# Optimization experiments

Measured on AMD Instinct MI355X. Metric: run time of the kernel, lower is better.

The kernel has to match this reference:

```python
import jax, jax.numpy as jnp
import numpy as np

H = 256  # hidden size for both encoder and decoder

def gru_cell(x, h, Wih, Whh, bih, bhh):
    # PyTorch nn.GRU cell: gates ordered (r, z, n)
    gi = x @ Wih.T + bih            # [N, 3H]
    gh = h @ Whh.T + bhh            # [N, 3H]
    ir, iz, inn = jnp.split(gi, 3, axis=-1)
    hr, hz, hn = jnp.split(gh, 3, axis=-1)
    r = jax.nn.sigmoid(ir + hr)
    z = jax.nn.sigmoid(iz + hz)
    n = jnp.tanh(inn + r * hn)
    return (1.0 - z) * n + z * h


def setup_inputs() -> dict:
    key = jax.random.key(0)
    ks = jax.random.split(key, 16)
    s = 0.05
    inp = {
        'x': jax.random.normal(ks[0], (32768, 15, 4), jnp.float32),
        'enc_embed_W': jax.random.normal(ks[1], (H, 4), jnp.float32) * s,
        'enc_embed_b': jax.random.normal(ks[2], (H,), jnp.float32) * s,
        'enc_Wih': jax.random.normal(ks[3], (3 * H, H), jnp.float32) * s,
        'enc_Whh': jax.random.normal(ks[4], (3 * H, H), jnp.float32) * s,
        'enc_bih': jax.random.normal(ks[5], (3 * H,), jnp.float32) * s,
        'enc_bhh': jax.random.normal(ks[6], (3 * H,), jnp.float32) * s,
        'dec_embed_W': jax.random.normal(ks[7], (H, H), jnp.float32) * s,
        'dec_embed_b': jax.random.normal(ks[8], (H,), jnp.float32) * s,
        'dec_Wih': jax.random.normal(ks[9], (3 * H, H), jnp.float32) * s,
        'dec_Whh': jax.random.normal(ks[10], (3 * H, H), jnp.float32) * s,
        'dec_bih': jax.random.normal(ks[11], (3 * H,), jnp.float32) * s,
        'dec_bhh': jax.random.normal(ks[12], (3 * H,), jnp.float32) * s,
        'out_W': jax.random.normal(ks[13], (4, H), jnp.float32) * s,
        'out_b': jax.random.normal(ks[14], (4,), jnp.float32) * s,
        'pred_len': 45,
    }
    return inp


def reference(x, enc_embed_W, enc_embed_b, enc_Wih, enc_Whh, enc_bih, enc_bhh,
              dec_embed_W, dec_embed_b, dec_Wih, dec_Whh, dec_bih, dec_bhh,
              out_W, out_b, pred_len):
    N = x.shape[0]
    # enc_embed: Linear + ReLU
    traj_feats = jax.nn.relu(jnp.einsum('nti,hi->nth', x, enc_embed_W) + enc_embed_b)
    # Encoder GRU over time (batch_first); we only need the final hidden state.
    h0 = jnp.zeros((N, H), x.dtype)

    def enc_step(h, xt):
        h = gru_cell(xt, h, enc_Wih, enc_Whh, enc_bih, enc_bhh)
        return h, None

    h_enc, _ = jax.lax.scan(enc_step, h0, jnp.swapaxes(traj_feats, 0, 1))

    dec_in0 = jax.nn.relu(h_enc @ dec_embed_W.T + dec_embed_b)

    def dec_step(carry, _):
        h, dec_in = carry
        h = gru_cell(dec_in, h, dec_Wih, dec_Whh, dec_bih, dec_bhh)
        out_t = h @ out_W.T + out_b                     # [N, 4]
        dec_in = jax.nn.relu(h @ dec_embed_W.T + dec_embed_b)
        return (h, dec_in), out_t

    _, outs = jax.lax.scan(dec_step, (h_enc, dec_in0), None, length=pred_len)
    return jnp.swapaxes(outs, 0, 1)  # [N, pred_len, 4]
```

## Files before the change

kernel.cpp:

```cpp
#include <hip/hip_runtime.h>
#include <hip/hip_bf16.h>
#include <hip/hip_fp16.h>

#define HD    256
#define TENC  15
#define PLEN  45
#define MROW  64
#define NTHR  512
#define NBLK  (32768 / MROW)

typedef __attribute__((ext_vector_type(16))) float f32x16;
typedef __attribute__((ext_vector_type(8)))  short bf16x8;

#define MFMA32 __builtin_amdgcn_mfma_f32_32x32x16_bf16

__device__ __forceinline__ unsigned short f2bf(float f) {
    union { float f; unsigned int u; } v; v.f = f;
    unsigned int r = v.u + 0x7FFF + ((v.u >> 16) & 1);
    return (unsigned short)(r >> 16);
}

__device__ __forceinline__ float fast_sig(float x) {
    float e = __builtin_amdgcn_exp2f(-1.44269504088896f * x);
    return __builtin_amdgcn_rcpf(1.f + e);
}
__device__ __forceinline__ float fast_tanh(float x) {
    float e = __builtin_amdgcn_exp2f(-2.88539008177793f * x);
    return (1.f - e) * __builtin_amdgcn_rcpf(1.f + e);
}

__global__ void xpose_w_kernel(const float* __restrict__ src,
                               unsigned short* __restrict__ dst, int n_gcols) {
    int t = blockIdx.x * blockDim.x + threadIdx.x;
    if (t >= n_gcols * 32) return;
    int gcol = t >> 5, c8 = t & 31;
    int kk = c8 >> 1, hi = c8 & 1;
    const float* s = src + (size_t)gcol * HD + c8 * 8;
    int seg = gcol >> 8, gc = gcol & 255;
    size_t d = (size_t)seg * 65536 +
               ((size_t)(((gc >> 5) * 16 + kk) * 64 + hi * 32 + (gc & 31))) * 8;
    unsigned short v[8];
    #pragma unroll
    for (int e = 0; e < 8; ++e) v[e] = f2bf(s[e]);
    *(bf16x8*)(dst + d) = *(bf16x8*)v;
}

__global__ void xpose_ow_kernel(const float* __restrict__ src,
                                unsigned short* __restrict__ dst) {
    int t = blockIdx.x * blockDim.x + threadIdx.x;
    if (t >= 32 * 32) return;
    int gcol = t >> 5, c8 = t & 31;
    int kk = c8 >> 1, hi = c8 & 1;
    unsigned short v[8];
    if (gcol < 4) {
        const float* s = src + (size_t)gcol * HD + c8 * 8;
        #pragma unroll
        for (int e = 0; e < 8; ++e) v[e] = f2bf(s[e]);
    } else {
        #pragma unroll
        for (int e = 0; e < 8; ++e) v[e] = 0;
    }
    size_t d = ((size_t)(kk * 64 + hi * 32 + gcol)) * 8;
    *(bf16x8*)(dst + d) = *(bf16x8*)v;
}

__device__ __forceinline__ int swz(int row, int col) {
    return row * 512 + ((((col >> 3) ^ row) & 31) << 4) + ((col & 7) << 1);
}

__global__ __launch_bounds__(NTHR, 2) void gru_main(
    const float* __restrict__ x,
    const float* __restrict__ eW, const float* __restrict__ eb,
    const unsigned short* __restrict__ encWih, const unsigned short* __restrict__ encWhh,
    const float* __restrict__ enc_bih, const float* __restrict__ enc_bhh,
    const unsigned short* __restrict__ decEW, const float* __restrict__ dec_eb,
    const unsigned short* __restrict__ decWih, const unsigned short* __restrict__ decWhh,
    const float* __restrict__ dec_bih, const float* __restrict__ dec_bhh,
    const unsigned short* __restrict__ outWt, const float* __restrict__ outb,
    float* __restrict__ out)
{
    __shared__ __align__(16) unsigned short ls_a[MROW * HD];
    __shared__ __align__(16) unsigned short ls_h[MROW * HD];
    __shared__ float ls_ew[HD * 4];
    __shared__ float ls_eb[HD];
    __shared__ float ls_bias[4 * HD];
    __shared__ float ls_deb[HD];

    const int tid   = threadIdx.x;
    const int lane  = tid & 63;
    const int wv    = tid >> 6;
    const int rowA  = lane & 31;
    const int hi    = lane >> 5;
    const int col   = wv * 32 + rowA;
    const int nbase = blockIdx.x * MROW;

    for (int i = tid; i < HD * 4; i += NTHR) ls_ew[i] = eW[i];
    if (tid < HD) {
        ls_eb[tid]            = eb[tid];
        ls_bias[tid]          = enc_bih[tid] + enc_bhh[tid];
        ls_bias[HD + tid]     = enc_bih[HD + tid] + enc_bhh[HD + tid];
        ls_bias[2 * HD + tid] = enc_bih[2 * HD + tid];
        ls_bias[3 * HD + tid] = enc_bhh[2 * HD + tid];
    }
    for (int i = tid; i < MROW * HD / 2; i += NTHR) ((unsigned int*)ls_h)[i] = 0u;

    __half2 hpk[16];
    #pragma unroll
    for (int i = 0; i < 16; ++i) hpk[i] = __floats2half2_rn(0.f, 0.f);

    float bR, bZ, bN, bH;

    f32x16 accR0, accR1, accZ0, accZ1, accN10, accN11, accN20, accN21;

    const char* pa = (const char*)ls_a + rowA * 512;
    const char* ph = (const char*)ls_h + rowA * 512;

    auto bcast = [](float v) {
        f32x16 a;
        #pragma unroll
        for (int i = 0; i < 16; ++i) a[i] = v;
        return a;
    };

    auto gates = [&](const unsigned short* Wi, const unsigned short* Wh) {
        accR0 = bcast(bR);  accR1 = accR0;
        accZ0 = bcast(bZ);  accZ1 = accZ0;
        accN10 = bcast(bN); accN11 = accN10;
        accN20 = bcast(bH); accN21 = accN20;
        const unsigned short* bi = Wi + wv * 8192 + lane * 8;
        const unsigned short* bh = Wh + wv * 8192 + lane * 8;
        #pragma unroll 2
        for (int kk = 0; kk < 16; ++kk) {
            const int sh = (((kk * 2 + hi) ^ rowA) & 31) << 4;
            bf16x8 ax0 = *(const bf16x8*)(pa + sh);
            bf16x8 ax1 = *(const bf16x8*)(pa + 16384 + sh);
            bf16x8 ah0 = *(const bf16x8*)(ph + sh);
            bf16x8 ah1 = *(const bf16x8*)(ph + 16384 + sh);
            const unsigned short* ki = bi + kk * 512;
            const unsigned short* kh = bh + kk * 512;
            bf16x8 bri = *(const bf16x8*)(ki);
            bf16x8 bzi = *(const bf16x8*)(ki + 65536);
            bf16x8 bni = *(const bf16x8*)(ki + 131072);
            bf16x8 brh = *(const bf16x8*)(kh);
            bf16x8 bzh = *(const bf16x8*)(kh + 65536);
            bf16x8 bnh = *(const bf16x8*)(kh + 131072);
            accR0  = MFMA32(ax0, bri, accR0, 0, 0, 0);
            accR1  = MFMA32(ax1, bri, accR1, 0, 0, 0);
            accZ0  = MFMA32(ax0, bzi, accZ0, 0, 0, 0);
            accZ1  = MFMA32(ax1, bzi, accZ1, 0, 0, 0);
            accN10 = MFMA32(ax0, bni, accN10, 0, 0, 0);
            accN11 = MFMA32(ax1, bni, accN11, 0, 0, 0);
            accR0  = MFMA32(ah0, brh, accR0, 0, 0, 0);
            accR1  = MFMA32(ah1, brh, accR1, 0, 0, 0);
            accZ0  = MFMA32(ah0, bzh, accZ0, 0, 0, 0);
            accZ1  = MFMA32(ah1, bzh, accZ1, 0, 0, 0);
            accN20 = MFMA32(ah0, bnh, accN20, 0, 0, 0);
            accN21 = MFMA32(ah1, bnh, accN21, 0, 0, 0);
        }
    };

    auto upd_tile = [&](f32x16& aR, f32x16& aZ, f32x16& aN1, f32x16& aN2, int rt) {
        #pragma unroll
        for (int q = 0; q < 16; q += 2) {
            float2 hv = __half22float2(hpk[rt * 8 + (q >> 1)]);
            float r0 = fast_sig(aR[q]);
            float z0 = fast_sig(aZ[q]);
            float n0 = fast_tanh(fmaf(r0, aN2[q], aN1[q]));
            float h0 = fmaf(z0, hv.x - n0, n0);
            float r1 = fast_sig(aR[q + 1]);
            float z1 = fast_sig(aZ[q + 1]);
            float n1 = fast_tanh(fmaf(r1, aN2[q + 1], aN1[q + 1]));
            float h1 = fmaf(z1, hv.y - n1, n1);
            hpk[rt * 8 + (q >> 1)] = __floats2half2_rn(h0, h1);
        }
    };

    auto write_h = [&]() {
        #pragma unroll
        for (int rt = 0; rt < 2; ++rt)
            #pragma unroll
            for (int q = 0; q < 16; q += 2) {
                float2 hv = __half22float2(hpk[rt * 8 + (q >> 1)]);
                int row = rt * 32 + (q & 3) + ((q >> 2) << 3) + (hi << 2);
                *(unsigned short*)((char*)ls_h + swz(row, col))     = f2bf(hv.x);
                *(unsigned short*)((char*)ls_h + swz(row + 1, col)) = f2bf(hv.y);
            }
    };

    auto embed_step = [&](int t) {
        int row = tid & 63;
        int c0  = (tid >> 6) * 32;
        const float4 xv = *(const float4*)(x + ((size_t)(nbase + row) * TENC + t) * 4);
        #pragma unroll 8
        for (int j = 0; j < 32; ++j) {
            int c = c0 + j;
            const float* wp = &ls_ew[c * 4];
            float v = fmaf(xv.x, wp[0], fmaf(xv.y, wp[1],
                      fmaf(xv.z, wp[2], fmaf(xv.w, wp[3], ls_eb[c]))));
            *(unsigned short*)((char*)ls_a + swz(row, c)) = f2bf(fmaxf(v, 0.f));
        }
    };

    float deb;

    auto dec_embed = [&]() {
        f32x16 o0 = bcast(deb), o1 = o0;
        const unsigned short* be = decEW + wv * 8192 + lane * 8;
        #pragma unroll 2
        for (int kk = 0; kk < 16; ++kk) {
            const int sh = (((kk * 2 + hi) ^ rowA) & 31) << 4;
            bf16x8 a0 = *(const bf16x8*)(ph + sh);
            bf16x8 a1 = *(const bf16x8*)(ph + 16384 + sh);
            bf16x8 b = *(const bf16x8*)(be + kk * 512);
            o0 = MFMA32(a0, b, o0, 0, 0, 0);
            o1 = MFMA32(a1, b, o1, 0, 0, 0);
        }
        #pragma unroll
        for (int rt = 0; rt < 2; ++rt) {
            const f32x16& o = rt ? o1 : o0;
            #pragma unroll
            for (int q = 0; q < 16; ++q) {
                int row = rt * 32 + (q & 3) + ((q >> 2) << 3) + (hi << 2);
                *(unsigned short*)((char*)ls_a + swz(row, col)) =
                    f2bf(fmaxf(o[q], 0.f));
            }
        }
    };

    float bb;

    auto out_layer = [&](int t) {
        if ((wv & 3) == 0) {
            const int rt = wv >> 2;
            f32x16 o = bcast(bb);
            const unsigned short* bo = outWt + lane * 8;
            #pragma unroll 2
            for (int kk = 0; kk < 16; ++kk) {
                const int sh = (((kk * 2 + hi) ^ rowA) & 31) << 4;
                bf16x8 a = *(const bf16x8*)(ph + rt * 16384 + sh);
                bf16x8 b = *(const bf16x8*)(bo + kk * 512);
                o = MFMA32(a, b, o, 0, 0, 0);
            }
            if (rowA < 4) {
                #pragma unroll
                for (int q = 0; q < 16; ++q) {
                    int row = rt * 32 + (q & 3) + ((q >> 2) << 3) + (hi << 2);
                    out[((size_t)(nbase + row) * PLEN + t) * 4 + rowA] = o[q];
                }
            }
        }
    };

    __syncthreads();
    bR = ls_bias[col];
    bZ = ls_bias[HD + col];
    bN = ls_bias[2 * HD + col];
    bH = ls_bias[3 * HD + col];
    embed_step(0);
    __syncthreads();

    for (int t = 0; t < TENC; ++t) {
        gates(encWih, encWhh);
        upd_tile(accR0, accZ0, accN10, accN20, 0);
        upd_tile(accR1, accZ1, accN11, accN21, 1);
        __syncthreads();
        write_h();
        if (t + 1 < TENC) embed_step(t + 1);
        __syncthreads();
    }

    if (tid < HD) {
        ls_bias[tid]          = dec_bih[tid] + dec_bhh[tid];
        ls_bias[HD + tid]     = dec_bih[HD + tid] + dec_bhh[HD + tid];
        ls_bias[2 * HD + tid] = dec_bih[2 * HD + tid];
        ls_bias[3 * HD + tid] = dec_bhh[2 * HD + tid];
        ls_deb[tid]           = dec_eb[tid];
    }
    __syncthreads();
    bR = ls_bias[col];
    bZ = ls_bias[HD + col];
    bN = ls_bias[2 * HD + col];
    bH = ls_bias[3 * HD + col];
    deb = ls_deb[col];
    bb  = (rowA < 4) ? outb[rowA] : 0.f;
    dec_embed();
    __syncthreads();

    for (int t = 0; t < PLEN; ++t) {
        gates(decWih, decWhh);
        upd_tile(accR0, accZ0, accN10, accN20, 0);
        upd_tile(accR1, accZ1, accN11, accN21, 1);
        __syncthreads();
        write_h();
        __syncthreads();
        dec_embed();
        __syncthreads();
        out_layer(t);
    }
}

extern "C" void kernel_launch(void* const* d_in, const int* in_sizes, int n_in,
                              void* d_out, int out_size, void* d_ws, size_t ws_size,
                              hipStream_t stream) {
    const float* x       = (const float*)d_in[0];
    const float* eW      = (const float*)d_in[1];
    const float* eb      = (const float*)d_in[2];
    const float* encWihf = (const float*)d_in[3];
    const float* encWhhf = (const float*)d_in[4];
    const float* enc_bih = (const float*)d_in[5];
    const float* enc_bhh = (const float*)d_in[6];
    const float* decEWf  = (const float*)d_in[7];
    const float* dec_eb  = (const float*)d_in[8];
    const float* decWihf = (const float*)d_in[9];
    const float* decWhhf = (const float*)d_in[10];
    const float* dec_bih = (const float*)d_in[11];
    const float* dec_bhh = (const float*)d_in[12];
    const float* outW    = (const float*)d_in[13];
    const float* outb    = (const float*)d_in[14];

    unsigned short* ws = (unsigned short*)d_ws;
    unsigned short* bWih_e = ws;
    unsigned short* bWhh_e = ws + 196608;
    unsigned short* bWih_d = ws + 2 * 196608;
    unsigned short* bWhh_d = ws + 3 * 196608;
    unsigned short* bEW_d  = ws + 4 * 196608;
    unsigned short* bOWt   = ws + 4 * 196608 + 65536;

    const int t1 = 768 * 32;
    const int t2 = 256 * 32;
    xpose_w_kernel<<<(t1 + 255) / 256, 256, 0, stream>>>(encWihf, bWih_e, 768);
    xpose_w_kernel<<<(t1 + 255) / 256, 256, 0, stream>>>(encWhhf, bWhh_e, 768);
    xpose_w_kernel<<<(t1 + 255) / 256, 256, 0, stream>>>(decWihf, bWih_d, 768);
    xpose_w_kernel<<<(t1 + 255) / 256, 256, 0, stream>>>(decWhhf, bWhh_d, 768);
    xpose_w_kernel<<<(t2 + 255) / 256, 256, 0, stream>>>(decEWf,  bEW_d,  256);
    xpose_ow_kernel<<<4, 256, 0, stream>>>(outW, bOWt);

    gru_main<<<NBLK, NTHR, 0, stream>>>(
        x, eW, eb, bWih_e, bWhh_e, enc_bih, enc_bhh,
        bEW_d, dec_eb, bWih_d, bWhh_d, dec_bih, dec_bhh,
        bOWt, outb, (float*)d_out);
}
```

Baseline: 2.279 ms.

## Double rows per block, split gate GEMMs into two passes, switch to fp16 MFMA

Each block now handles 128 rows instead of 64, so each weight fragment loaded from global memory feeds four MFMA row tiles instead of two. To hold the larger tile within registers, the gate computation is split into two passes: the first computes r and the hidden-side n term, combined in a mid step, and the second computes z and the input-side n term. Weights and activations move from bf16 to fp16, which removes the manual bf16 rounding and lets h be written straight from its half-packed registers. The cost is twice the LDS per block, half as many blocks, reuse of the A operands across both passes, and fp16 range limits.

```diff
diff --git a/kernel.cpp b/kernel.cpp
--- a/kernel.cpp
+++ b/kernel.cpp
@@ -5,20 +5,14 @@
 #define HD    256
 #define TENC  15
 #define PLEN  45
-#define MROW  64
+#define MROW  128
 #define NTHR  512
 #define NBLK  (32768 / MROW)
 
-typedef __attribute__((ext_vector_type(16))) float f32x16;
-typedef __attribute__((ext_vector_type(8)))  short bf16x8;
-
-#define MFMA32 __builtin_amdgcn_mfma_f32_32x32x16_bf16
-
-__device__ __forceinline__ unsigned short f2bf(float f) {
-    union { float f; unsigned int u; } v; v.f = f;
-    unsigned int r = v.u + 0x7FFF + ((v.u >> 16) & 1);
-    return (unsigned short)(r >> 16);
-}
+typedef __attribute__((ext_vector_type(16))) float     f32x16;
+typedef __attribute__((ext_vector_type(8)))  _Float16  f16x8;
+
+#define MFMAH __builtin_amdgcn_mfma_f32_32x32x16_f16
 
 __device__ __forceinline__ float fast_sig(float x) {
     float e = __builtin_amdgcn_exp2f(-1.44269504088896f * x);
@@ -30,7 +24,7 @@
 }
 
 __global__ void xpose_w_kernel(const float* __restrict__ src,
-                               unsigned short* __restrict__ dst, int n_gcols) {
+                               _Float16* __restrict__ dst, int n_gcols) {
     int t = blockIdx.x * blockDim.x + threadIdx.x;
     if (t >= n_gcols * 32) return;
     int gcol = t >> 5, c8 = t & 31;
@@ -39,29 +33,29 @@
     int seg = gcol >> 8, gc = gcol & 255;
     size_t d = (size_t)seg * 65536 +
                ((size_t)(((gc >> 5) * 16 + kk) * 64 + hi * 32 + (gc & 31))) * 8;
-    unsigned short v[8];
+    _Float16 v[8];
     #pragma unroll
-    for (int e = 0; e < 8; ++e) v[e] = f2bf(s[e]);
-    *(bf16x8*)(dst + d) = *(bf16x8*)v;
+    for (int e = 0; e < 8; ++e) v[e] = (_Float16)s[e];
+    *(f16x8*)(dst + d) = *(f16x8*)v;
 }
 
 __global__ void xpose_ow_kernel(const float* __restrict__ src,
-                                unsigned short* __restrict__ dst) {
+                                _Float16* __restrict__ dst) {
     int t = blockIdx.x * blockDim.x + threadIdx.x;
     if (t >= 32 * 32) return;
     int gcol = t >> 5, c8 = t & 31;
     int kk = c8 >> 1, hi = c8 & 1;
-    unsigned short v[8];
+    _Float16 v[8];
     if (gcol < 4) {
         const float* s = src + (size_t)gcol * HD + c8 * 8;
         #pragma unroll
-        for (int e = 0; e < 8; ++e) v[e] = f2bf(s[e]);
+        for (int e = 0; e < 8; ++e) v[e] = (_Float16)s[e];
     } else {
         #pragma unroll
-        for (int e = 0; e < 8; ++e) v[e] = 0;
+        for (int e = 0; e < 8; ++e) v[e] = (_Float16)0.f;
     }
     size_t d = ((size_t)(kk * 64 + hi * 32 + gcol)) * 8;
-    *(bf16x8*)(dst + d) = *(bf16x8*)v;
+    *(f16x8*)(dst + d) = *(f16x8*)v;
 }
 
 __device__ __forceinline__ int swz(int row, int col) {
@@ -71,16 +65,16 @@
 __global__ __launch_bounds__(NTHR, 2) void gru_main(
     const float* __restrict__ x,
     const float* __restrict__ eW, const float* __restrict__ eb,
-    const unsigned short* __restrict__ encWih, const unsigned short* __restrict__ encWhh,
+    const _Float16* __restrict__ encWih, const _Float16* __restrict__ encWhh,
     const float* __restrict__ enc_bih, const float* __restrict__ enc_bhh,
-    const unsigned short* __restrict__ decEW, const float* __restrict__ dec_eb,
-    const unsigned short* __restrict__ decWih, const unsigned short* __restrict__ decWhh,
+    const _Float16* __restrict__ decEW, const float* __restrict__ dec_eb,
+    const _Float16* __restrict__ decWih, const _Float16* __restrict__ decWhh,
     const float* __restrict__ dec_bih, const float* __restrict__ dec_bhh,
-    const unsigned short* __restrict__ outWt, const float* __restrict__ outb,
+    const _Float16* __restrict__ outWt, const float* __restrict__ outb,
     float* __restrict__ out)
 {
-    __shared__ __align__(16) unsigned short ls_a[MROW * HD];
-    __shared__ __align__(16) unsigned short ls_h[MROW * HD];
+    __shared__ __align__(16) char ls_a[MROW * 512];
+    __shared__ __align__(16) char ls_h[MROW * 512];
     __shared__ float ls_ew[HD * 4];
     __shared__ float ls_eb[HD];
     __shared__ float ls_bias[4 * HD];
@@ -102,18 +96,18 @@
         ls_bias[2 * HD + tid] = enc_bih[2 * HD + tid];
         ls_bias[3 * HD + tid] = enc_bhh[2 * HD + tid];
     }
-    for (int i = tid; i < MROW * HD / 2; i += NTHR) ((unsigned int*)ls_h)[i] = 0u;
-
-    __half2 hpk[16];
+    for (int i = tid; i < MROW * 512 / 4; i += NTHR) ((unsigned int*)ls_h)[i] = 0u;
+
+    __half2 hpk[32];
     #pragma unroll
-    for (int i = 0; i < 16; ++i) hpk[i] = __floats2half2_rn(0.f, 0.f);
+    for (int i = 0; i < 32; ++i) hpk[i] = __floats2half2_rn(0.f, 0.f);
 
     float bR, bZ, bN, bH;
 
-    f32x16 accR0, accR1, accZ0, accZ1, accN10, accN11, accN20, accN21;
-
-    const char* pa = (const char*)ls_a + rowA * 512;
-    const char* ph = (const char*)ls_h + rowA * 512;
+    f32x16 accA[4], accB[4];
+
+    const char* pa = ls_a + rowA * 512;
+    const char* ph = ls_h + rowA * 512;
 
     auto bcast = [](float v) {
         f32x16 a;
@@ -122,124 +116,167 @@
         return a;
     };
 
-    auto gates = [&](const unsigned short* Wi, const unsigned short* Wh) {
-        accR0 = bcast(bR);  accR1 = accR0;
-        accZ0 = bcast(bZ);  accZ1 = accZ0;
-        accN10 = bcast(bN); accN11 = accN10;
-        accN20 = bcast(bH); accN21 = accN20;
-        const unsigned short* bi = Wi + wv * 8192 + lane * 8;
-        const unsigned short* bh = Wh + wv * 8192 + lane * 8;
-        #pragma unroll 2
+    auto pass1 = [&](const _Float16* Wi, const _Float16* Wh) {
+        #pragma unroll
+        for (int rt = 0; rt < 4; ++rt) { accA[rt] = bcast(bR); accB[rt] = bcast(bH); }
+        const _Float16* bi = Wi + wv * 8192 + lane * 8;
+        const _Float16* bh = Wh + wv * 8192 + lane * 8;
+        #pragma unroll 4
         for (int kk = 0; kk < 16; ++kk) {
             const int sh = (((kk * 2 + hi) ^ rowA) & 31) << 4;
-            bf16x8 ax0 = *(const bf16x8*)(pa + sh);
-            bf16x8 ax1 = *(const bf16x8*)(pa + 16384 + sh);
-            bf16x8 ah0 = *(const bf16x8*)(ph + sh);
-            bf16x8 ah1 = *(const bf16x8*)(ph + 16384 + sh);
-            const unsigned short* ki = bi + kk * 512;
-            const unsigned short* kh = bh + kk * 512;
-            bf16x8 bri = *(const bf16x8*)(ki);
-            bf16x8 bzi = *(const bf16x8*)(ki + 65536);
-            bf16x8 bni = *(const bf16x8*)(ki + 131072);
-            bf16x8 brh = *(const bf16x8*)(kh);
-            bf16x8 bzh = *(const bf16x8*)(kh + 65536);
-            bf16x8 bnh = *(const bf16x8*)(kh + 131072);
-            accR0  = MFMA32(ax0, bri, accR0, 0, 0, 0);
-            accR1  = MFMA32(ax1, bri, accR1, 0, 0, 0);
-            accZ0  = MFMA32(ax0, bzi, accZ0, 0, 0, 0);
-            accZ1  = MFMA32(ax1, bzi, accZ1, 0, 0, 0);
-            accN10 = MFMA32(ax0, bni, accN10, 0, 0, 0);
-            accN11 = MFMA32(ax1, bni, accN11, 0, 0, 0);
-            accR0  = MFMA32(ah0, brh, accR0, 0, 0, 0);
-            accR1  = MFMA32(ah1, brh, accR1, 0, 0, 0);
-            accZ0  = MFMA32(ah0, bzh, accZ0, 0, 0, 0);
-            accZ1  = MFMA32(ah1, bzh, accZ1, 0, 0, 0);
-            accN20 = MFMA32(ah0, bnh, accN20, 0, 0, 0);
-            accN21 = MFMA32(ah1, bnh, accN21, 0, 0, 0);
-        }
-    };
-
-    auto upd_tile = [&](f32x16& aR, f32x16& aZ, f32x16& aN1, f32x16& aN2, int rt) {
-        #pragma unroll
-        for (int q = 0; q < 16; q += 2) {
-            float2 hv = __half22float2(hpk[rt * 8 + (q >> 1)]);
-            float r0 = fast_sig(aR[q]);
-            float z0 = fast_sig(aZ[q]);
-            float n0 = fast_tanh(fmaf(r0, aN2[q], aN1[q]));
-            float h0 = fmaf(z0, hv.x - n0, n0);
-            float r1 = fast_sig(aR[q + 1]);
-            float z1 = fast_sig(aZ[q + 1]);
-            float n1 = fast_tanh(fmaf(r1, aN2[q + 1], aN1[q + 1]));
-            float h1 = fmaf(z1, hv.y - n1, n1);
-            hpk[rt * 8 + (q >> 1)] = __floats2half2_rn(h0, h1);
-        }
-    };
-
-    auto write_h = [&]() {
-        #pragma unroll
-        for (int rt = 0; rt < 2; ++rt)
+            f16x8 ax0 = *(const f16x8*)(pa + sh);
+            f16x8 ax1 = *(const f16x8*)(pa + 16384 + sh);
+            f16x8 ax2 = *(const f16x8*)(pa + 32768 + sh);
+            f16x8 ax3 = *(const f16x8*)(pa + 49152 + sh);
+            f16x8 ah0 = *(const f16x8*)(ph + sh);
+            f16x8 ah1 = *(const f16x8*)(ph + 16384 + sh);
+            f16x8 ah2 = *(const f16x8*)(ph + 32768 + sh);
+            f16x8 ah3 = *(const f16x8*)(ph + 49152 + sh);
+            f16x8 bri = *(const f16x8*)(bi + kk * 512);
+            f16x8 brh = *(const f16x8*)(bh + kk * 512);
+            f16x8 bnh = *(const f16x8*)(bh + kk * 512 + 131072);
+            accA[0] = MFMAH(ax0, bri, accA[0], 0, 0, 0);
+            accA[1] = MFMAH(ax1, bri, accA[1], 0, 0, 0);
+            accA[2] = MFMAH(ax2, bri, accA[2], 0, 0, 0);
+            accA[3] = MFMAH(ax3, bri, accA[3], 0, 0, 0);
+            accA[0] = MFMAH(ah0, brh, accA[0], 0, 0, 0);
+            accA[1] = MFMAH(ah1, brh, accA[1], 0, 0, 0);
+            accA[2] = MFMAH(ah2, brh, accA[2], 0, 0, 0);
+            accA[3] = MFMAH(ah3, brh, accA[3], 0, 0, 0);
+            accB[0] = MFMAH(ah0, bnh, accB[0], 0, 0, 0);
+            accB[1] = MFMAH(ah1, bnh, accB[1], 0, 0, 0);
+            accB[2] = MFMAH(ah2, bnh, accB[2], 0, 0, 0);
+            accB[3] = MFMAH(ah3, bnh, accB[3], 0, 0, 0);
+        }
+    };
+
+    auto mid = [&]() {
+        #pragma unroll
+        for (int rt = 0; rt < 4; ++rt)
+            #pragma unroll
+            for (int q = 0; q < 16; ++q) {
+                float rr = fast_sig(accA[rt][q]);
+                accB[rt][q] = fmaf(rr, accB[rt][q], bN);
+            }
+    };
+
+    auto pass2 = [&](const _Float16* Wi, const _Float16* Wh) {
+        #pragma unroll
+        for (int rt = 0; rt < 4; ++rt) accA[rt] = bcast(bZ);
+        const _Float16* bi = Wi + wv * 8192 + lane * 8;
+        const _Float16* bh = Wh + wv * 8192 + lane * 8;
+        #pragma unroll 4
+        for (int kk = 0; kk < 16; ++kk) {
+            const int sh = (((kk * 2 + hi) ^ rowA) & 31) << 4;
+            f16x8 ax0 = *(const f16x8*)(pa + sh);
+            f16x8 ax1 = *(const f16x8*)(pa + 16384 + sh);
+            f16x8 ax2 = *(const f16x8*)(pa + 32768 + sh);
+            f16x8 ax3 = *(const f16x8*)(pa + 49152 + sh);
+            f16x8 ah0 = *(const f16x8*)(ph + sh);
+            f16x8 ah1 = *(const f16x8*)(ph + 16384 + sh);
+            f16x8 ah2 = *(const f16x8*)(ph + 32768 + sh);
+            f16x8 ah3 = *(const f16x8*)(ph + 49152 + sh);
+            f16x8 bzi = *(const f16x8*)(bi + kk * 512 + 65536);
+            f16x8 bzh = *(const f16x8*)(bh + kk * 512 + 65536);
+            f16x8 bni = *(const f16x8*)(bi + kk * 512 + 131072);
+            accA[0] = MFMAH(ax0, bzi, accA[0], 0, 0, 0);
+            accA[1] = MFMAH(ax1, bzi, accA[1], 0, 0, 0);
+            accA[2] = MFMAH(ax2, bzi, accA[2], 0, 0, 0);
+            accA[3] = MFMAH(ax3, bzi, accA[3], 0, 0, 0);
+            accA[0] = MFMAH(ah0, bzh, accA[0], 0, 0, 0);
+            accA[1] = MFMAH(ah1, bzh, accA[1], 0, 0, 0);
+            accA[2] = MFMAH(ah2, bzh, accA[2], 0, 0, 0);
+            accA[3] = MFMAH(ah3, bzh, accA[3], 0, 0, 0);
+            accB[0] = MFMAH(ax0, bni, accB[0], 0, 0, 0);
+            accB[1] = MFMAH(ax1, bni, accB[1], 0, 0, 0);
+            accB[2] = MFMAH(ax2, bni, accB[2], 0, 0, 0);
+            accB[3] = MFMAH(ax3, bni, accB[3], 0, 0, 0);
+        }
+    };
+
+    auto final_upd = [&]() {
+        #pragma unroll
+        for (int rt = 0; rt < 4; ++rt)
             #pragma unroll
             for (int q = 0; q < 16; q += 2) {
                 float2 hv = __half22float2(hpk[rt * 8 + (q >> 1)]);
+                float z0 = fast_sig(accA[rt][q]);
+                float n0 = fast_tanh(accB[rt][q]);
+                float h0 = fmaf(z0, hv.x - n0, n0);
+                float z1 = fast_sig(accA[rt][q + 1]);
+                float n1 = fast_tanh(accB[rt][q + 1]);
+                float h1 = fmaf(z1, hv.y - n1, n1);
+                hpk[rt * 8 + (q >> 1)] = __floats2half2_rn(h0, h1);
+            }
+    };
+
+    auto write_h = [&]() {
+        #pragma unroll
+        for (int rt = 0; rt < 4; ++rt)
+            #pragma unroll
+            for (int q = 0; q < 16; q += 2) {
+                unsigned int u = *(unsigned int*)&hpk[rt * 8 + (q >> 1)];
                 int row = rt * 32 + (q & 3) + ((q >> 2) << 3) + (hi << 2);
-                *(unsigned short*)((char*)ls_h + swz(row, col))     = f2bf(hv.x);
-                *(unsigned short*)((char*)ls_h + swz(row + 1, col)) = f2bf(hv.y);
+                *(unsigned short*)(ls_h + swz(row, col))     = (unsigned short)u;
+                *(unsigned short*)(ls_h + swz(row + 1, col)) = (unsigned short)(u >> 16);
             }
     };
 
     auto embed_step = [&](int t) {
-        int row = tid & 63;
-        int c0  = (tid >> 6) * 32;
+        int row = tid & 127;
+        int c0  = (tid >> 7) * 64;
         const float4 xv = *(const float4*)(x + ((size_t)(nbase + row) * TENC + t) * 4);
         #pragma unroll 8
-        for (int j = 0; j < 32; ++j) {
+        for (int j = 0; j < 64; ++j) {
             int c = c0 + j;
             const float* wp = &ls_ew[c * 4];
             float v = fmaf(xv.x, wp[0], fmaf(xv.y, wp[1],
                       fmaf(xv.z, wp[2], fmaf(xv.w, wp[3], ls_eb[c]))));
-            *(unsigned short*)((char*)ls_a + swz(row, c)) = f2bf(fmaxf(v, 0.f));
+            *(_Float16*)(ls_a + swz(row, c)) = (_Float16)fmaxf(v, 0.f);
         }
     };
 
     float deb;
+    float bb;
 
     auto dec_embed = [&]() {
-        f32x16 o0 = bcast(deb), o1 = o0;
-        const unsigned short* be = decEW + wv * 8192 + lane * 8;
-        #pragma unroll 2
+        f32x16 o0 = bcast(deb), o1 = o0, o2 = o0, o3 = o0;
+        const _Float16* be = decEW + wv * 8192 + lane * 8;
+        #pragma unroll 4
         for (int kk = 0; kk < 16; ++kk) {
             const int sh = (((kk * 2 + hi) ^ rowA) & 31) << 4;
-            bf16x8 a0 = *(const bf16x8*)(ph + sh);
-            bf16x8 a1 = *(const bf16x8*)(ph + 16384 + sh);
-            bf16x8 b = *(const bf16x8*)(be + kk * 512);
-            o0 = MFMA32(a0, b, o0, 0, 0, 0);
-            o1 = MFMA32(a1, b, o1, 0, 0, 0);
-        }
-        #pragma unroll
-        for (int rt = 0; rt < 2; ++rt) {
-            const f32x16& o = rt ? o1 : o0;
+            f16x8 a0 = *(const f16x8*)(ph + sh);
+            f16x8 a1 = *(const f16x8*)(ph + 16384 + sh);
+            f16x8 a2 = *(const f16x8*)(ph + 32768 + sh);
+            f16x8 a3 = *(const f16x8*)(ph + 49152 + sh);
+            f16x8 b = *(const f16x8*)(be + kk * 512);
+            o0 = MFMAH(a0, b, o0, 0, 0, 0);
+            o1 = MFMAH(a1, b, o1, 0, 0, 0);
+            o2 = MFMAH(a2, b, o2, 0, 0, 0);
+            o3 = MFMAH(a3, b, o3, 0, 0, 0);
+        }
+        #pragma unroll
+        for (int rt = 0; rt < 4; ++rt) {
+            const f32x16& o = rt == 0 ? o0 : rt == 1 ? o1 : rt == 2 ? o2 : o3;
             #pragma unroll
             for (int q = 0; q < 16; ++q) {
                 int row = rt * 32 + (q & 3) + ((q >> 2) << 3) + (hi << 2);
-                *(unsigned short*)((char*)ls_a + swz(row, col)) =
-                    f2bf(fmaxf(o[q], 0.f));
-            }
-        }
-    };
-
-    float bb;
+                *(_Float16*)(ls_a + swz(row, col)) = (_Float16)fmaxf(o[q], 0.f);
+            }
+        }
+    };
 
     auto out_layer = [&](int t) {
-        if ((wv & 3) == 0) {
-            const int rt = wv >> 2;
+        if ((wv & 1) == 0) {
+            const int rt = wv >> 1;
             f32x16 o = bcast(bb);
-            const unsigned short* bo = outWt + lane * 8;
-            #pragma unroll 2
+            const _Float16* bo = outWt + lane * 8;
+            #pragma unroll 4
             for (int kk = 0; kk < 16; ++kk) {
                 const int sh = (((kk * 2 + hi) ^ rowA) & 31) << 4;
-                bf16x8 a = *(const bf16x8*)(ph + rt * 16384 + sh);
-                bf16x8 b = *(const bf16x8*)(bo + kk * 512);
-                o = MFMA32(a, b, o, 0, 0, 0);
+                f16x8 a = *(const f16x8*)(ph + rt * 16384 + sh);
+                f16x8 b = *(const f16x8*)(bo + kk * 512);
+                o = MFMAH(a, b, o, 0, 0, 0);
             }
             if (rowA < 4) {
                 #pragma unroll
@@ -260,9 +297,10 @@
     __syncthreads();
 
     for (int t = 0; t < TENC; ++t) {
-        gates(encWih, encWhh);
-        upd_tile(accR0, accZ0, accN10, accN20, 0);
-        upd_tile(accR1, accZ1, accN11, accN21, 1);
+        pass1(encWih, encWhh);
+        mid();
+        pass2(encWih, encWhh);
+        final_upd();
         __syncthreads();
         write_h();
         if (t + 1 < TENC) embed_step(t + 1);
@@ -287,9 +325,10 @@
     __syncthreads();
 
     for (int t = 0; t < PLEN; ++t) {
-        gates(decWih, decWhh);
-        upd_tile(accR0, accZ0, accN10, accN20, 0);
-        upd_tile(accR1, accZ1, accN11, accN21, 1);
+        pass1(decWih, decWhh);
+        mid();
+        pass2(decWih, decWhh);
+        final_upd();
         __syncthreads();
         write_h();
         __syncthreads();
@@ -318,25 +357,25 @@
     const float* outW    = (const float*)d_in[13];
     const float* outb    = (const float*)d_in[14];
 
-    unsigned short* ws = (unsigned short*)d_ws;
-    unsigned short* bWih_e = ws;
-    unsigned short* bWhh_e = ws + 196608;
-    unsigned short* bWih_d = ws + 2 * 196608;
-    unsigned short* bWhh_d = ws + 3 * 196608;
-    unsigned short* bEW_d  = ws + 4 * 196608;
-    unsigned short* bOWt   = ws + 4 * 196608 + 65536;
+    _Float16* ws = (_Float16*)d_ws;
+    _Float16* hWih_e = ws;
+    _Float16* hWhh_e = ws + 196608;
+    _Float16* hWih_d = ws + 2 * 196608;
+    _Float16* hWhh_d = ws + 3 * 196608;
+    _Float16* hEW_d  = ws + 4 * 196608;
+    _Float16* hOWt   = ws + 4 * 196608 + 65536;
 
     const int t1 = 768 * 32;
     const int t2 = 256 * 32;
-    xpose_w_kernel<<<(t1 + 255) / 256, 256, 0, stream>>>(encWihf, bWih_e, 768);
-    xpose_w_kernel<<<(t1 + 255) / 256, 256, 0, stream>>>(encWhhf, bWhh_e, 768);
-    xpose_w_kernel<<<(t1 + 255) / 256, 256, 0, stream>>>(decWihf, bWih_d, 768);
-    xpose_w_kernel<<<(t1 + 255) / 256, 256, 0, stream>>>(decWhhf, bWhh_d, 768);
-    xpose_w_kernel<<<(t2 + 255) / 256, 256, 0, stream>>>(decEWf,  bEW_d,  256);
-    xpose_ow_kernel<<<4, 256, 0, stream>>>(outW, bOWt);
+    xpose_w_kernel<<<(t1 + 255) / 256, 256, 0, stream>>>(encWihf, hWih_e, 768);
+    xpose_w_kernel<<<(t1 + 255) / 256, 256, 0, stream>>>(encWhhf, hWhh_e, 768);
+    xpose_w_kernel<<<(t1 + 255) / 256, 256, 0, stream>>>(decWihf, hWih_d, 768);
+    xpose_w_kernel<<<(t1 + 255) / 256, 256, 0, stream>>>(decWhhf, hWhh_d, 768);
+    xpose_w_kernel<<<(t2 + 255) / 256, 256, 0, stream>>>(decEWf,  hEW_d,  256);
+    xpose_ow_kernel<<<4, 256, 0, stream>>>(outW, hOWt);
 
     gru_main<<<NBLK, NTHR, 0, stream>>>(
-        x, eW, eb, bWih_e, bWhh_e, enc_bih, enc_bhh,
-        bEW_d, dec_eb, bWih_d, bWhh_d, dec_bih, dec_bhh,
-        bOWt, outb, (float*)d_out);
-}
+        x, eW, eb, hWih_e, hWhh_e, enc_bih, enc_bhh,
+        hEW_d, dec_eb, hWih_d, hWhh_d, dec_bih, dec_bhh,
+        hOWt, outb, (float*)d_out);
+}
```

Result: slower. 3.409 ms (+49.6%).

## Switch GRU MFMAs to fp16 and double-buffer LDS activations to drop barriers

Applied to the files above, without the earlier changes.

Replaces bf16 weights and MFMAs with fp16, so the fp16-packed hidden state can be stored to LDS directly without a bf16 conversion. Adds ping-pong buffers for the input and hidden tiles in LDS, so the new hidden state is written without waiting for all warps to finish reading the old one. This removes one __syncthreads per encoder and decoder step. It doubles LDS use, which may cut the number of resident blocks per CU, and fp16 narrows the exponent range compared with bf16.

```diff
diff --git a/kernel.cpp b/kernel.cpp
--- a/kernel.cpp
+++ b/kernel.cpp
@@ -1,5 +1,4 @@
 #include <hip/hip_runtime.h>
-#include <hip/hip_bf16.h>
 #include <hip/hip_fp16.h>
 
 #define HD    256
@@ -9,16 +8,10 @@
 #define NTHR  512
 #define NBLK  (32768 / MROW)
 
-typedef __attribute__((ext_vector_type(16))) float f32x16;
-typedef __attribute__((ext_vector_type(8)))  short bf16x8;
-
-#define MFMA32 __builtin_amdgcn_mfma_f32_32x32x16_bf16
-
-__device__ __forceinline__ unsigned short f2bf(float f) {
-    union { float f; unsigned int u; } v; v.f = f;
-    unsigned int r = v.u + 0x7FFF + ((v.u >> 16) & 1);
-    return (unsigned short)(r >> 16);
-}
+typedef __attribute__((ext_vector_type(16))) float     f32x16;
+typedef __attribute__((ext_vector_type(8)))  _Float16  f16x8;
+
+#define MFMAH __builtin_amdgcn_mfma_f32_32x32x16_f16
 
 __device__ __forceinline__ float fast_sig(float x) {
     float e = __builtin_amdgcn_exp2f(-1.44269504088896f * x);
@@ -30,7 +23,7 @@
 }
 
 __global__ void xpose_w_kernel(const float* __restrict__ src,
-                               unsigned short* __restrict__ dst, int n_gcols) {
+                               _Float16* __restrict__ dst, int n_gcols) {
     int t = blockIdx.x * blockDim.x + threadIdx.x;
     if (t >= n_gcols * 32) return;
     int gcol = t >> 5, c8 = t & 31;
@@ -39,29 +32,29 @@
     int seg = gcol >> 8, gc = gcol & 255;
     size_t d = (size_t)seg * 65536 +
                ((size_t)(((gc >> 5) * 16 + kk) * 64 + hi * 32 + (gc & 31))) * 8;
-    unsigned short v[8];
+    _Float16 v[8];
     #pragma unroll
-    for (int e = 0; e < 8; ++e) v[e] = f2bf(s[e]);
-    *(bf16x8*)(dst + d) = *(bf16x8*)v;
+    for (int e = 0; e < 8; ++e) v[e] = (_Float16)s[e];
+    *(f16x8*)(dst + d) = *(f16x8*)v;
 }
 
 __global__ void xpose_ow_kernel(const float* __restrict__ src,
-                                unsigned short* __restrict__ dst) {
+                                _Float16* __restrict__ dst) {
     int t = blockIdx.x * blockDim.x + threadIdx.x;
     if (t >= 32 * 32) return;
     int gcol = t >> 5, c8 = t & 31;
     int kk = c8 >> 1, hi = c8 & 1;
-    unsigned short v[8];
+    _Float16 v[8];
     if (gcol < 4) {
         const float* s = src + (size_t)gcol * HD + c8 * 8;
         #pragma unroll
-        for (int e = 0; e < 8; ++e) v[e] = f2bf(s[e]);
+        for (int e = 0; e < 8; ++e) v[e] = (_Float16)s[e];
     } else {
         #pragma unroll
-        for (int e = 0; e < 8; ++e) v[e] = 0;
+        for (int e = 0; e < 8; ++e) v[e] = (_Float16)0.f;
     }
     size_t d = ((size_t)(kk * 64 + hi * 32 + gcol)) * 8;
-    *(bf16x8*)(dst + d) = *(bf16x8*)v;
+    *(f16x8*)(dst + d) = *(f16x8*)v;
 }
 
 __device__ __forceinline__ int swz(int row, int col) {
@@ -71,16 +64,16 @@
 __global__ __launch_bounds__(NTHR, 2) void gru_main(
     const float* __restrict__ x,
     const float* __restrict__ eW, const float* __restrict__ eb,
-    const unsigned short* __restrict__ encWih, const unsigned short* __restrict__ encWhh,
+    const _Float16* __restrict__ encWih, const _Float16* __restrict__ encWhh,
     const float* __restrict__ enc_bih, const float* __restrict__ enc_bhh,
-    const unsigned short* __restrict__ decEW, const float* __restrict__ dec_eb,
-    const unsigned short* __restrict__ decWih, const unsigned short* __restrict__ decWhh,
+    const _Float16* __restrict__ decEW, const float* __restrict__ dec_eb,
+    const _Float16* __restrict__ decWih, const _Float16* __restrict__ decWhh,
     const float* __restrict__ dec_bih, const float* __restrict__ dec_bhh,
-    const unsigned short* __restrict__ outWt, const float* __restrict__ outb,
+    const _Float16* __restrict__ outWt, const float* __restrict__ outb,
     float* __restrict__ out)
 {
-    __shared__ __align__(16) unsigned short ls_a[MROW * HD];
-    __shared__ __align__(16) unsigned short ls_h[MROW * HD];
+    __shared__ __align__(16) char ls_a[2][MROW * 512];
+    __shared__ __align__(16) char ls_h[2][MROW * 512];
     __shared__ float ls_ew[HD * 4];
     __shared__ float ls_eb[HD];
     __shared__ float ls_bias[4 * HD];
@@ -102,18 +95,16 @@
         ls_bias[2 * HD + tid] = enc_bih[2 * HD + tid];
         ls_bias[3 * HD + tid] = enc_bhh[2 * HD + tid];
     }
-    for (int i = tid; i < MROW * HD / 2; i += NTHR) ((unsigned int*)ls_h)[i] = 0u;
+    for (int i = tid; i < MROW * 512 / 4; i += NTHR) ((unsigned int*)ls_h[0])[i] = 0u;
 
     __half2 hpk[16];
     #pragma unroll
     for (int i = 0; i < 16; ++i) hpk[i] = __floats2half2_rn(0.f, 0.f);
 
     float bR, bZ, bN, bH;
+    float deb, bb;
 
     f32x16 accR0, accR1, accZ0, accZ1, accN10, accN11, accN20, accN21;
-
-    const char* pa = (const char*)ls_a + rowA * 512;
-    const char* ph = (const char*)ls_h + rowA * 512;
 
     auto bcast = [](float v) {
         f32x16 a;
@@ -122,40 +113,42 @@
         return a;
     };
 
-    auto gates = [&](const unsigned short* Wi, const unsigned short* Wh) {
+    auto gates = [&](const _Float16* Wi, const _Float16* Wh, int ar, int hr) {
         accR0 = bcast(bR);  accR1 = accR0;
         accZ0 = bcast(bZ);  accZ1 = accZ0;
         accN10 = bcast(bN); accN11 = accN10;
         accN20 = bcast(bH); accN21 = accN20;
-        const unsigned short* bi = Wi + wv * 8192 + lane * 8;
-        const unsigned short* bh = Wh + wv * 8192 + lane * 8;
+        const char* pA = ls_a[ar] + rowA * 512;
+        const char* pH = ls_h[hr] + rowA * 512;
+        const _Float16* bi = Wi + wv * 8192 + lane * 8;
+        const _Float16* bh = Wh + wv * 8192 + lane * 8;
         #pragma unroll 2
         for (int kk = 0; kk < 16; ++kk) {
             const int sh = (((kk * 2 + hi) ^ rowA) & 31) << 4;
-            bf16x8 ax0 = *(const bf16x8*)(pa + sh);
-            bf16x8 ax1 = *(const bf16x8*)(pa + 16384 + sh);
-            bf16x8 ah0 = *(const bf16x8*)(ph + sh);
-            bf16x8 ah1 = *(const bf16x8*)(ph + 16384 + sh);
-            const unsigned short* ki = bi + kk * 512;
-            const unsigned short* kh = bh + kk * 512;
-            bf16x8 bri = *(const bf16x8*)(ki);
-            bf16x8 bzi = *(const bf16x8*)(ki + 65536);
-            bf16x8 bni = *(const bf16x8*)(ki + 131072);
-            bf16x8 brh = *(const bf16x8*)(kh);
-            bf16x8 bzh = *(const bf16x8*)(kh + 65536);
-            bf16x8 bnh = *(const bf16x8*)(kh + 131072);
-            accR0  = MFMA32(ax0, bri, accR0, 0, 0, 0);
-            accR1  = MFMA32(ax1, bri, accR1, 0, 0, 0);
-            accZ0  = MFMA32(ax0, bzi, accZ0, 0, 0, 0);
-            accZ1  = MFMA32(ax1, bzi, accZ1, 0, 0, 0);
-            accN10 = MFMA32(ax0, bni, accN10, 0, 0, 0);
-            accN11 = MFMA32(ax1, bni, accN11, 0, 0, 0);
-            accR0  = MFMA32(ah0, brh, accR0, 0, 0, 0);
-            accR1  = MFMA32(ah1, brh, accR1, 0, 0, 0);
-            accZ0  = MFMA32(ah0, bzh, accZ0, 0, 0, 0);
-            accZ1  = MFMA32(ah1, bzh, accZ1, 0, 0, 0);
-            accN20 = MFMA32(ah0, bnh, accN20, 0, 0, 0);
-            accN21 = MFMA32(ah1, bnh, accN21, 0, 0, 0);
+            f16x8 ax0 = *(const f16x8*)(pA + sh);
+            f16x8 ax1 = *(const f16x8*)(pA + 16384 + sh);
+            f16x8 ah0 = *(const f16x8*)(pH + sh);
+            f16x8 ah1 = *(const f16x8*)(pH + 16384 + sh);
+            const _Float16* ki = bi + kk * 512;
+            const _Float16* kh = bh + kk * 512;
+            f16x8 bri = *(const f16x8*)(ki);
+            f16x8 bzi = *(const f16x8*)(ki + 65536);
+            f16x8 bni = *(const f16x8*)(ki + 131072);
+            f16x8 brh = *(const f16x8*)(kh);
+            f16x8 bzh = *(const f16x8*)(kh + 65536);
+            f16x8 bnh = *(const f16x8*)(kh + 131072);
+            accR0  = MFMAH(ax0, bri, accR0, 0, 0, 0);
+            accR1  = MFMAH(ax1, bri, accR1, 0, 0, 0);
+            accZ0  = MFMAH(ax0, bzi, accZ0, 0, 0, 0);
+            accZ1  = MFMAH(ax1, bzi, accZ1, 0, 0, 0);
+            accN10 = MFMAH(ax0, bni, accN10, 0, 0, 0);
+            accN11 = MFMAH(ax1, bni, accN11, 0, 0, 0);
+            accR0  = MFMAH(ah0, brh, accR0, 0, 0, 0);
+            accR1  = MFMAH(ah1, brh, accR1, 0, 0, 0);
+            accZ0  = MFMAH(ah0, bzh, accZ0, 0, 0, 0);
+            accZ1  = MFMAH(ah1, bzh, accZ1, 0, 0, 0);
+            accN20 = MFMAH(ah0, bnh, accN20, 0, 0, 0);
+            accN21 = MFMAH(ah1, bnh, accN21, 0, 0, 0);
         }
     };
 
@@ -175,19 +168,19 @@
         }
     };
 
-    auto write_h = [&]() {
+    auto write_h = [&](int hw) {
         #pragma unroll
         for (int rt = 0; rt < 2; ++rt)
             #pragma unroll
             for (int q = 0; q < 16; q += 2) {
-                float2 hv = __half22float2(hpk[rt * 8 + (q >> 1)]);
+                unsigned int u = *(unsigned int*)&hpk[rt * 8 + (q >> 1)];
                 int row = rt * 32 + (q & 3) + ((q >> 2) << 3) + (hi << 2);
-                *(unsigned short*)((char*)ls_h + swz(row, col))     = f2bf(hv.x);
-                *(unsigned short*)((char*)ls_h + swz(row + 1, col)) = f2bf(hv.y);
+                *(unsigned short*)(ls_h[hw] + swz(row, col))     = (unsigned short)u;
+                *(unsigned short*)(ls_h[hw] + swz(row + 1, col)) = (unsigned short)(u >> 16);
             }
     };
 
-    auto embed_step = [&](int t) {
+    auto embed_step = [&](int t, int aw) {
         int row = tid & 63;
         int c0  = (tid >> 6) * 32;
         const float4 xv = *(const float4*)(x + ((size_t)(nbase + row) * TENC + t) * 4);
@@ -197,23 +190,22 @@
             const float* wp = &ls_ew[c * 4];
             float v = fmaf(xv.x, wp[0], fmaf(xv.y, wp[1],
                       fmaf(xv.z, wp[2], fmaf(xv.w, wp[3], ls_eb[c]))));
-            *(unsigned short*)((char*)ls_a + swz(row, c)) = f2bf(fmaxf(v, 0.f));
-        }
-    };
-
-    float deb;
-
-    auto dec_embed = [&]() {
+            *(_Float16*)(ls_a[aw] + swz(row, c)) = (_Float16)fmaxf(v, 0.f);
+        }
+    };
+
+    auto dec_embed = [&](int hr, int aw) {
         f32x16 o0 = bcast(deb), o1 = o0;
-        const unsigned short* be = decEW + wv * 8192 + lane * 8;
+        const char* pH = ls_h[hr] + rowA * 512;
+        const _Float16* be = decEW + wv * 8192 + lane * 8;
         #pragma unroll 2
         for (int kk = 0; kk < 16; ++kk) {
             const int sh = (((kk * 2 + hi) ^ rowA) & 31) << 4;
-            bf16x8 a0 = *(const bf16x8*)(ph + sh);
-            bf16x8 a1 = *(const bf16x8*)(ph + 16384 + sh);
-            bf16x8 b = *(const bf16x8*)(be + kk * 512);
-            o0 = MFMA32(a0, b, o0, 0, 0, 0);
-            o1 = MFMA32(a1, b, o1, 0, 0, 0);
+            f16x8 a0 = *(const f16x8*)(pH + sh);
+            f16x8 a1 = *(const f16x8*)(pH + 16384 + sh);
+            f16x8 b = *(const f16x8*)(be + kk * 512);
+            o0 = MFMAH(a0, b, o0, 0, 0, 0);
+            o1 = MFMAH(a1, b, o1, 0, 0, 0);
         }
         #pragma unroll
         for (int rt = 0; rt < 2; ++rt) {
@@ -221,25 +213,23 @@
             #pragma unroll
             for (int q = 0; q < 16; ++q) {
                 int row = rt * 32 + (q & 3) + ((q >> 2) << 3) + (hi << 2);
-                *(unsigned short*)((char*)ls_a + swz(row, col)) =
-                    f2bf(fmaxf(o[q], 0.f));
+                *(_Float16*)(ls_a[aw] + swz(row, col)) = (_Float16)fmaxf(o[q], 0.f);
             }
         }
     };
 
-    float bb;
-
-    auto out_layer = [&](int t) {
+    auto out_layer = [&](int t, int hr) {
         if ((wv & 3) == 0) {
             const int rt = wv >> 2;
             f32x16 o = bcast(bb);
-            const unsigned short* bo = outWt + lane * 8;
+            const char* pH = ls_h[hr] + rowA * 512 + rt * 16384;
+            const _Float16* bo = outWt + lane * 8;
             #pragma unroll 2
             for (int kk = 0; kk < 16; ++kk) {
                 const int sh = (((kk * 2 + hi) ^ rowA) & 31) << 4;
-                bf16x8 a = *(const bf16x8*)(ph + rt * 16384 + sh);
-                bf16x8 b = *(const bf16x8*)(bo + kk * 512);
-                o = MFMA32(a, b, o, 0, 0, 0);
+                f16x8 a = *(const f16x8*)(pH + sh);
+                f16x8 b = *(const f16x8*)(bo + kk * 512);
+                o = MFMAH(a, b, o, 0, 0, 0);
             }
             if (rowA < 4) {
                 #pragma unroll
@@ -256,17 +246,19 @@
     bZ = ls_bias[HD + col];
     bN = ls_bias[2 * HD + col];
     bH = ls_bias[3 * HD + col];
-    embed_step(0);
+    embed_step(0, 0);
     __syncthreads();
 
+    int ac = 0, hc = 0;
+
     for (int t = 0; t < TENC; ++t) {
-        gates(encWih, encWhh);
+        gates(encWih, encWhh, ac, hc);
         upd_tile(accR0, accZ0, accN10, accN20, 0);
         upd_tile(accR1, accZ1, accN11, accN21, 1);
+        write_h(hc ^ 1);
+        if (t + 1 < TENC) embed_step(t + 1, ac ^ 1);
         __syncthreads();
-        write_h();
-        if (t + 1 < TENC) embed_step(t + 1);
-        __syncthreads();
+        ac ^= 1; hc ^= 1;
     }
 
     if (tid < HD) {
@@ -283,19 +275,20 @@
     bH = ls_bias[3 * HD + col];
     deb = ls_deb[col];
     bb  = (rowA < 4) ? outb[rowA] : 0.f;
-    dec_embed();
+    ac = 0;
+    dec_embed(hc, ac);
     __syncthreads();
 
     for (int t = 0; t < PLEN; ++t) {
-        gates(decWih, decWhh);
+        gates(decWih, decWhh, ac, hc);
         upd_tile(accR0, accZ0, accN10, accN20, 0);
         upd_tile(accR1, accZ1, accN11, accN21, 1);
+        write_h(hc ^ 1);
         __syncthreads();
-        write_h();
+        dec_embed(hc ^ 1, ac ^ 1);
         __syncthreads();
-        dec_embed();
-        __syncthreads();
-        out_layer(t);
+        out_layer(t, hc ^ 1);
+        ac ^= 1; hc ^= 1;
     }
 }
 
@@ -318,25 +311,25 @@
     const float* outW    = (const float*)d_in[13];
     const float* outb    = (const float*)d_in[14];
 
-    unsigned short* ws = (unsigned short*)d_ws;
-    unsigned short* bWih_e = ws;
-    unsigned short* bWhh_e = ws + 196608;
-    unsigned short* bWih_d = ws + 2 * 196608;
-    unsigned short* bWhh_d = ws + 3 * 196608;
-    unsigned short* bEW_d  = ws + 4 * 196608;
-    unsigned short* bOWt   = ws + 4 * 196608 + 65536;
+    _Float16* ws = (_Float16*)d_ws;
+    _Float16* hWih_e = ws;
+    _Float16* hWhh_e = ws + 196608;
+    _Float16* hWih_d = ws + 2 * 196608;
+    _Float16* hWhh_d = ws + 3 * 196608;
+    _Float16* hEW_d  = ws + 4 * 196608;
+    _Float16* hOWt   = ws + 4 * 196608 + 65536;
 
     const int t1 = 768 * 32;
     const int t2 = 256 * 32;
-    xpose_w_kernel<<<(t1 + 255) / 256, 256, 0, stream>>>(encWihf, bWih_e, 768);
-    xpose_w_kernel<<<(t1 + 255) / 256, 256, 0, stream>>>(encWhhf, bWhh_e, 768);
-    xpose_w_kernel<<<(t1 + 255) / 256, 256, 0, stream>>>(decWihf, bWih_d, 768);
-    xpose_w_kernel<<<(t1 + 255) / 256, 256, 0, stream>>>(decWhhf, bWhh_d, 768);
-    xpose_w_kernel<<<(t2 + 255) / 256, 256, 0, stream>>>(decEWf,  bEW_d,  256);
-    xpose_ow_kernel<<<4, 256, 0, stream>>>(outW, bOWt);
+    xpose_w_kernel<<<(t1 + 255) / 256, 256, 0, stream>>>(encWihf, hWih_e, 768);
+    xpose_w_kernel<<<(t1 + 255) / 256, 256, 0, stream>>>(encWhhf, hWhh_e, 768);
+    xpose_w_kernel<<<(t1 + 255) / 256, 256, 0, stream>>>(decWihf, hWih_d, 768);
+    xpose_w_kernel<<<(t1 + 255) / 256, 256, 0, stream>>>(decWhhf, hWhh_d, 768);
+    xpose_w_kernel<<<(t2 + 255) / 256, 256, 0, stream>>>(decEWf,  hEW_d,  256);
+    xpose_ow_kernel<<<4, 256, 0, stream>>>(outW, hOWt);
 
     gru_main<<<NBLK, NTHR, 0, stream>>>(
-        x, eW, eb, bWih_e, bWhh_e, enc_bih, enc_bhh,
-        bEW_d, dec_eb, bWih_d, bWhh_d, dec_bih, dec_bhh,
-        bOWt, outb, (float*)d_out);
-}
+        x, eW, eb, hWih_e, hWhh_e, enc_bih, enc_bhh,
+        hEW_d, dec_eb, hWih_d, hWhh_d, dec_bih, dec_bhh,
+        hOWt, outb, (float*)d_out);
+}
```

Measured after the change: 2.297 ms. Within noise of the previous version (+0.8%).
